# Performance work log

Hardware: AMD Instinct MI355X
Metric: run time of the kernel (lower is better)

The kernel has to match this reference:

```python
import jax, jax.numpy as jnp
import numpy as np

# dims: L = 1 + H*W tokens (cls first), BT = B*T clips*frames
L, BT, D = 577, 128, 768
B, T = 16, 8
H = W = 24
CM = 192   # d_middle = D // REDUCTION(4)
CR = 48    # CM // rf_r(4)
K = 3      # rf_k and spatial kernel


def setup_inputs() -> dict:
    key = jax.random.key(0)
    ks = jax.random.split(key, 10)
    return {
        "x":      jax.random.normal(ks[0], (L, BT, D), jnp.float32),
        # tada_pre_proj: Linear(D -> CM)
        "w_pre":  jax.random.normal(ks[1], (D, CM), jnp.float32) * 0.02,
        "b_pre":  jnp.zeros((CM,), jnp.float32),
        # TAdaConv2dV2 base depthwise weight (1x3x3, groups=CM) and bias
        "w_base": jax.random.normal(ks[2], (K, K, 1, CM), jnp.float32) * 0.1,
        "b_conv": jnp.zeros((CM,), jnp.float32),
        # route function: global 1x1 branch, temporal conv a (CM->CR), temporal conv b (CR->CM, small init)
        "w_g":    jax.random.normal(ks[3], (CM, CM), jnp.float32) * 0.02,
        "b_g":    jnp.zeros((CM,), jnp.float32),
        "w_a":    jax.random.normal(ks[4], (K, CM, CR), jnp.float32) * 0.05,
        "b_a":    jnp.zeros((CR,), jnp.float32),
        "w_b":    jax.random.normal(ks[5], (K, CR, CM), jnp.float32) * 0.02,
        # tada_proj: Linear(CM -> D)
        "w_proj": jax.random.normal(ks[6], (CM, D), jnp.float32) * 0.02,
        "b_proj": jnp.zeros((D,), jnp.float32),
    }


def reference(x, w_pre, b_pre, w_base, b_conv, w_g, b_g, w_a, b_a, w_b, w_proj, b_proj):
    # --- tada_pre_proj ---
    h = x @ w_pre + b_pre                                   # [L, BT, CM]
    cls_tok, sp = h[:1], h[1:]                              # cls token bypasses the conv
    sp = sp.transpose(1, 0, 2).reshape(BT, H, W, CM)        # [BT, H, W, CM]

    # --- route function: per-frame, per-channel calibration alpha ---
    d = sp.reshape(B, T, H * W, CM).mean(axis=2)            # spatial avg pool -> [B, T, CM]
    g = d.mean(axis=1) @ w_g + b_g                          # global temporal descriptor [B, CM]
    a = jax.lax.conv_general_dilated(d + g[:, None, :], w_a, (1,), 'SAME',
                                     dimension_numbers=('NWC', 'WIO', 'NWC')) + b_a
    a = jax.nn.relu(a)                                      # [B, T, CR]
    alpha = jax.lax.conv_general_dilated(a, w_b, (1,), 'SAME',
                                         dimension_numbers=('NWC', 'WIO', 'NWC')) + 1.0  # [B, T, CM]

    # --- calibrated depthwise conv (cal_dim='cout') ---
    # conv2d(x, alpha * W_base) == alpha * conv2d(x, W_base) for depthwise cout calibration
    y = jax.lax.conv_general_dilated(sp, w_base, (1, 1), 'SAME',
                                     dimension_numbers=('NHWC', 'HWIO', 'NHWC'),
                                     feature_group_count=CM)
    y = y * alpha.reshape(BT, 1, 1, CM) + b_conv            # [BT, H, W, CM]
    y = y.reshape(BT, H * W, CM).transpose(1, 0, 2)         # [HW, BT, CM]
    out = jnp.concatenate([cls_tok, y], axis=0)             # [L, BT, CM]

    # --- QuickGELU + tada_proj ---
    out = out * jax.nn.sigmoid(1.702 * out)
    return out @ w_proj + b_proj                            # [L, BT, D]
```

## Files before the change

kernel.cpp:

```cpp
#include <hip/hip_runtime.h>

#define DEV __device__ __forceinline__

typedef short bf16x8 __attribute__((ext_vector_type(8)));
typedef float f32x4  __attribute__((ext_vector_type(4)));
typedef unsigned short ushort_t;


DEV unsigned short f2bf(float f) {
  unsigned u = __float_as_uint(f);
  unsigned r = (u + 0x7fffu + ((u >> 16) & 1u)) >> 16;
  return (unsigned short)r;
}

DEV unsigned cvt_pk_bf16(float a, float b) {
  unsigned r;
  asm("v_cvt_pk_bf16_f32 %0, %1, %2" : "=v"(r) : "v"(a), "v"(b));
  return r;
}

DEV float bf2f(unsigned short b) { return __uint_as_float((unsigned)b << 16); }

DEV float silu_g(float v) { return v / (1.f + __expf(-1.702f * v)); }

DEV void gload_lds16(const void* g, void* l) {
  __builtin_amdgcn_global_load_lds(
      (const __attribute__((address_space(1))) unsigned int*)g,
      (__attribute__((address_space(3))) unsigned int*)l, 16, 0, 0);
}

__global__ __launch_bounds__(256)
void prep_kernel(const float* __restrict__ w_pre, const float* __restrict__ w_proj,
                 short* __restrict__ w_preT, short* __restrict__ w_projT) {
  int i = blockIdx.x * 256 + threadIdx.x;
  if (i < 192 * 768) {
    int n = i / 768, k = i - n * 768;
    w_preT[i] = (short)f2bf(w_pre[k * 192 + n]);
    int n2 = i / 192, k2 = i - n2 * 192;
    w_projT[i] = (short)f2bf(w_proj[k2 * 768 + n2]);
  }
}

__global__ __launch_bounds__(512, 4)
void gemm1_kernel(const float* __restrict__ Af, const short* __restrict__ Bt,
                  const float* __restrict__ bias, ushort_t* __restrict__ C) {
  constexpr int BM = 128, BN = 192, BK = 64, KTOT = 768, NTOT = 192, NT = 12;
  __shared__ short As[2][BM * BK];
  __shared__ short Bs[2][BN * BK];

  const int tid  = threadIdx.x;
  const int wave = tid >> 6, lane = tid & 63;
  const int m0 = blockIdx.x * BM;
  const int wm = wave >> 2, wn = wave & 3;
  const int lr  = lane & 15;
  const int lk8 = lane >> 4;
  const int srow = lane >> 3;
  const int schunk = lane & 7;

  f32x4 acc[4][3] = {};
  float4 areg[2][2];

  auto loadA_f32 = [&](int kt) {
    #pragma unroll
    for (int s = 0; s < 2; ++s) {
      int id = tid + s * 512;
      int r = id >> 3, c = id & 7;
      int cg = c ^ (r & 7);
      const float* p = Af + (size_t)(m0 + r) * KTOT + kt + cg * 8;
      areg[s][0] = *(const float4*)p;
      areg[s][1] = *(const float4*)(p + 4);
    }
  };
  auto cvtStoreA = [&](int buf) {
    #pragma unroll
    for (int s = 0; s < 2; ++s) {
      int id = tid + s * 512;
      int r = id >> 3, c = id & 7;
      int4 w;
      w.x = (int)cvt_pk_bf16(areg[s][0].x, areg[s][0].y);
      w.y = (int)cvt_pk_bf16(areg[s][0].z, areg[s][0].w);
      w.z = (int)cvt_pk_bf16(areg[s][1].x, areg[s][1].y);
      w.w = (int)cvt_pk_bf16(areg[s][1].z, areg[s][1].w);
      *(int4*)&As[buf][r * 64 + c * 8] = w;
    }
  };
  auto stageB = [&](int kt, int buf) {
    #pragma unroll
    for (int j = 0; j < 3; ++j) {
      int rb8 = wave * 3 + j;
      int r = rb8 * 8 + srow;
      const short* src = Bt + (size_t)r * KTOT + kt + (schunk ^ srow) * 8;
      gload_lds16(src, (char*)Bs[buf] + rb8 * 1024);
    }
  };
  auto compute = [&](int buf) {
    #pragma unroll
    for (int ks = 0; ks < 2; ++ks) {
      int kc = ks * 4 + lk8;
      bf16x8 af[4], bfv[3];
      #pragma unroll
      for (int fm = 0; fm < 4; ++fm) {
        int row = wm * 64 + fm * 16 + lr;
        af[fm] = *(const bf16x8*)&As[buf][row * 64 + (kc ^ (row & 7)) * 8];
      }
      #pragma unroll
      for (int fn = 0; fn < 3; ++fn) {
        int row = wn * 48 + fn * 16 + lr;
        bfv[fn] = *(const bf16x8*)&Bs[buf][row * 64 + (kc ^ (row & 7)) * 8];
      }
      #pragma unroll
      for (int fm = 0; fm < 4; ++fm)
        #pragma unroll
        for (int fn = 0; fn < 3; ++fn)
          acc[fm][fn] = __builtin_amdgcn_mfma_f32_16x16x32_bf16(
              bfv[fn], af[fm], acc[fm][fn], 0, 0, 0);
    }
  };

  loadA_f32(0);
  cvtStoreA(0);
  stageB(0, 0);
  loadA_f32(BK);
  asm volatile("s_waitcnt vmcnt(4) lgkmcnt(0)" ::: "memory");
  __builtin_amdgcn_s_barrier();

  #pragma unroll
  for (int t = 0; t < NT; ++t) {
    const int cur = t & 1, nxt = cur ^ 1;
    if (t + 1 < NT) {
      stageB((t + 1) * BK, nxt);
      cvtStoreA(nxt);
      if (t + 2 < NT) loadA_f32((t + 2) * BK);
    }
    compute(cur);
    if (t + 1 < NT) {
      if (t + 2 < NT)
        asm volatile("s_waitcnt vmcnt(4) lgkmcnt(0)" ::: "memory");
      else
        asm volatile("s_waitcnt vmcnt(0) lgkmcnt(0)" ::: "memory");
      __builtin_amdgcn_s_barrier();
    }
  }

  const int cb = (lane >> 4) * 4;
  #pragma unroll
  for (int fm = 0; fm < 4; ++fm) {
    int row = m0 + wm * 64 + fm * 16 + lr;
    #pragma unroll
    for (int fn = 0; fn < 3; ++fn) {
      int col = wn * 48 + fn * 16 + cb;
      float4 bv = *(const float4*)(bias + col);
      int2 w;
      w.x = (int)cvt_pk_bf16(acc[fm][fn][0] + bv.x, acc[fm][fn][1] + bv.y);
      w.y = (int)cvt_pk_bf16(acc[fm][fn][2] + bv.z, acc[fm][fn][3] + bv.w);
      *(int2*)&C[(size_t)row * NTOT + col] = w;
    }
  }
}

__global__ __launch_bounds__(512)
void gemm2_kernel(const short* __restrict__ Ab, const short* __restrict__ Bt,
                  const float* __restrict__ bias, float* __restrict__ C) {
  constexpr int BM = 128, BN = 192, BK = 64, KTOT = 192, NTOT = 768;
  __shared__ short As[3][BM * BK];
  __shared__ short Bs[3][BN * BK];

  const int tid  = threadIdx.x;
  const int wave = tid >> 6, lane = tid & 63;
  const int m0 = blockIdx.x * BM;
  const int n0 = blockIdx.y * BN;
  const int wm = wave >> 2, wn = wave & 3;
  const int lr  = lane & 15;
  const int lk8 = lane >> 4;
  const int srow = lane >> 3;
  const int schunk = lane & 7;

  f32x4 acc[4][3] = {};

  #pragma unroll
  for (int tt = 0; tt < 3; ++tt) {
    int kt = tt * BK;
    #pragma unroll
    for (int j = 0; j < 2; ++j) {
      int rb8 = wave * 2 + j;
      int r = rb8 * 8 + srow;
      const short* src = Ab + (size_t)(m0 + r) * KTOT + kt + (schunk ^ srow) * 8;
      gload_lds16(src, (char*)As[tt] + rb8 * 1024);
    }
    #pragma unroll
    for (int j = 0; j < 3; ++j) {
      int rb8 = wave * 3 + j;
      int r = rb8 * 8 + srow;
      const short* src = Bt + (size_t)(n0 + r) * KTOT + kt + (schunk ^ srow) * 8;
      gload_lds16(src, (char*)Bs[tt] + rb8 * 1024);
    }
  }

  auto compute = [&](int buf) {
    #pragma unroll
    for (int ks = 0; ks < 2; ++ks) {
      int kc = ks * 4 + lk8;
      bf16x8 af[4], bfv[3];
      #pragma unroll
      for (int fm = 0; fm < 4; ++fm) {
        int row = wm * 64 + fm * 16 + lr;
        af[fm] = *(const bf16x8*)&As[buf][row * 64 + (kc ^ (row & 7)) * 8];
      }
      #pragma unroll
      for (int fn = 0; fn < 3; ++fn) {
        int row = wn * 48 + fn * 16 + lr;
        bfv[fn] = *(const bf16x8*)&Bs[buf][row * 64 + (kc ^ (row & 7)) * 8];
      }
      #pragma unroll
      for (int fm = 0; fm < 4; ++fm)
        #pragma unroll
        for (int fn = 0; fn < 3; ++fn)
          acc[fm][fn] = __builtin_amdgcn_mfma_f32_16x16x32_bf16(
              bfv[fn], af[fm], acc[fm][fn], 0, 0, 0);
    }
  };

  asm volatile("s_waitcnt vmcnt(10)" ::: "memory");
  __builtin_amdgcn_s_barrier();
  compute(0);
  asm volatile("s_waitcnt vmcnt(5)" ::: "memory");
  __builtin_amdgcn_s_barrier();
  compute(1);
  asm volatile("s_waitcnt vmcnt(0)" ::: "memory");
  __builtin_amdgcn_s_barrier();
  compute(2);

  const int cb = (lane >> 4) * 4;
  #pragma unroll
  for (int fm = 0; fm < 4; ++fm) {
    int row = m0 + wm * 64 + fm * 16 + lr;
    #pragma unroll
    for (int fn = 0; fn < 3; ++fn) {
      int col = n0 + wn * 48 + fn * 16 + cb;
      float4 bv = *(const float4*)(bias + col);
      f32x4 o;
      o[0] = acc[fm][fn][0] + bv.x;
      o[1] = acc[fm][fn][1] + bv.y;
      o[2] = acc[fm][fn][2] + bv.z;
      o[3] = acc[fm][fn][3] + bv.w;
      __builtin_nontemporal_store(o, (f32x4*)&C[(size_t)row * NTOT + col]);
    }
  }
}

__global__ __launch_bounds__(384)
void reduce_d_kernel(const ushort_t* __restrict__ h, float* __restrict__ d) {
  const int bt = blockIdx.x, tid = threadIdx.x;
  const int slice = tid / 24, c8 = tid % 24;
  __shared__ float part[16][192];
  float sum[8] = {};
  #pragma unroll 4
  for (int i = 0; i < 36; ++i) {
    int l = 1 + slice * 36 + i;
    bf16x8 v = *(const bf16x8*)&h[((size_t)l * 128 + bt) * 192 + c8 * 8];
    #pragma unroll
    for (int j = 0; j < 8; ++j) sum[j] += bf2f((unsigned short)v[j]);
  }
  #pragma unroll
  for (int j = 0; j < 8; ++j) part[slice][c8 * 8 + j] = sum[j];
  __syncthreads();
  if (tid < 192) {
    float s = 0.f;
    #pragma unroll
    for (int sl = 0; sl < 16; ++sl) s += part[sl][tid];
    d[bt * 192 + tid] = s * (1.f / 576.f);
  }
}

__global__ __launch_bounds__(256)
void small_path_kernel(const float* __restrict__ d,
                       const float* __restrict__ w_g, const float* __restrict__ b_g,
                       const float* __restrict__ w_a, const float* __restrict__ b_a,
                       const float* __restrict__ w_b,
                       float* __restrict__ alpha) {
  const int b = blockIdx.x, tid = threadIdx.x;
  __shared__ unsigned short wg_buf[36864];
  __shared__ unsigned short wa_buf[27648];
  __shared__ float e[8][192];
  __shared__ float md[192];
  __shared__ float a[8][48];

  #pragma unroll
  for (int it = 0; it < 36; ++it) {
    int i = tid + it * 256;
    float4 v = *(const float4*)(w_g + i * 4);
    int2 w;
    w.x = (int)cvt_pk_bf16(v.x, v.y);
    w.y = (int)cvt_pk_bf16(v.z, v.w);
    *(int2*)&wg_buf[i * 4] = w;
  }
  #pragma unroll
  for (int it = 0; it < 27; ++it) {
    int i = tid + it * 256;
    float4 v = *(const float4*)(w_a + i * 4);
    int2 w;
    w.x = (int)cvt_pk_bf16(v.x, v.y);
    w.y = (int)cvt_pk_bf16(v.z, v.w);
    *(int2*)&wa_buf[i * 4] = w;
  }
  for (int i = tid; i < 384; i += 256)
    *(float4*)((float*)e + i * 4) = *(const float4*)(d + (size_t)b * 1536 + i * 4);
  __syncthreads();

  if (tid < 192) {
    float m = 0.f;
    #pragma unroll
    for (int t = 0; t < 8; ++t) m += e[t][tid];
    md[tid] = m * 0.125f;
  }
  __syncthreads();

  if (tid < 192) {
    float accg = b_g[tid];
    #pragma unroll 8
    for (int k = 0; k < 192; ++k)
      accg += md[k] * bf2f(wg_buf[k * 192 + tid]);
    #pragma unroll
    for (int t = 0; t < 8; ++t) e[t][tid] += accg;
  }
  __syncthreads();

  #pragma unroll
  for (int it = 0; it < 27; ++it) {
    int i = tid + it * 256;
    float4 v = *(const float4*)(w_b + i * 4);
    int2 w;
    w.x = (int)cvt_pk_bf16(v.x, v.y);
    w.y = (int)cvt_pk_bf16(v.z, v.w);
    *(int2*)&wg_buf[i * 4] = w;
  }
  for (int o = tid; o < 384; o += 256) {
    int t = o / 48, r = o - t * 48;
    float acc = b_a[r];
    #pragma unroll
    for (int dt = 0; dt < 3; ++dt) {
      int tt = t + dt - 1;
      if ((unsigned)tt < 8u) {
        #pragma unroll 8
        for (int k = 0; k < 192; ++k)
          acc += e[tt][k] * bf2f(wa_buf[(dt * 192 + k) * 48 + r]);
      }
    }
    a[t][r] = fmaxf(acc, 0.f);
  }
  __syncthreads();

  if (tid < 192) {
    #pragma unroll
    for (int t = 0; t < 8; ++t) {
      float acc = 1.0f;
      #pragma unroll
      for (int dt = 0; dt < 3; ++dt) {
        int tt = t + dt - 1;
        if ((unsigned)tt < 8u) {
          #pragma unroll 8
          for (int r = 0; r < 48; ++r)
            acc += a[tt][r] * bf2f(wg_buf[(dt * 48 + r) * 192 + tid]);
        }
      }
      alpha[(size_t)(b * 8 + t) * 192 + tid] = acc;
    }
  }
}

__global__ __launch_bounds__(256)
void dwconv_silu_kernel(const ushort_t* __restrict__ h, const float* __restrict__ alpha,
                        const float* __restrict__ w_base, const float* __restrict__ b_conv,
                        ushort_t* __restrict__ s) {
  const int bt = blockIdx.x, c0 = blockIdx.y * 32;
  const int tid = threadIdx.x;
  __shared__ ushort_t tile[576][32];

  #pragma unroll
  for (int it = 0; it < 9; ++it) {
    int gidx = tid + it * 256;
    int p = gidx >> 2, cc = (gidx & 3) * 8;
    *(bf16x8*)&tile[p][cc] =
        *(const bf16x8*)&h[((size_t)(1 + p) * 128 + bt) * 192 + c0 + cc];
  }

  const int c = tid & 31;
  const int prow = tid >> 5;
  float wv[3][3];
  #pragma unroll
  for (int dh = 0; dh < 3; ++dh)
    #pragma unroll
    for (int dw = 0; dw < 3; ++dw)
      wv[dh][dw] = w_base[(dh * 3 + dw) * 192 + c0 + c];
  const float av = alpha[bt * 192 + c0 + c];
  const float bc = b_conv[c0 + c];

  if (tid < 32) {
    float v = bf2f(h[(size_t)bt * 192 + c0 + tid]);
    s[(size_t)bt * 192 + c0 + tid] = f2bf(silu_g(v));
  }
  __syncthreads();

  for (int i = 0; i < 72; ++i) {
    int p = prow + i * 8;
    int hh = p / 24, ww = p - hh * 24;
    float acc = 0.f;
    #pragma unroll
    for (int dh = 0; dh < 3; ++dh) {
      int y = hh + dh - 1;
      if ((unsigned)y >= 24u) continue;
      #pragma unroll
      for (int dw = 0; dw < 3; ++dw) {
        int xx = ww + dw - 1;
        if ((unsigned)xx >= 24u) continue;
        acc += bf2f(tile[y * 24 + xx][c]) * wv[dh][dw];
      }
    }
    float pre = acc * av + bc;
    s[(size_t)((1 + p) * 128 + bt) * 192 + c0 + c] = f2bf(silu_g(pre));
  }
}

extern "C" void kernel_launch(void* const* d_in, const int* in_sizes, int n_in,
                              void* d_out, int out_size, void* d_ws, size_t ws_size,
                              hipStream_t stream) {
  (void)in_sizes; (void)n_in; (void)out_size; (void)ws_size;
  const float* x      = (const float*)d_in[0];
  const float* w_pre  = (const float*)d_in[1];
  const float* b_pre  = (const float*)d_in[2];
  const float* w_base = (const float*)d_in[3];
  const float* b_conv = (const float*)d_in[4];
  const float* w_g    = (const float*)d_in[5];
  const float* b_g    = (const float*)d_in[6];
  const float* w_a    = (const float*)d_in[7];
  const float* b_a    = (const float*)d_in[8];
  const float* w_b    = (const float*)d_in[9];
  const float* w_proj = (const float*)d_in[10];
  const float* b_proj = (const float*)d_in[11];

  float* out = (float*)d_out;
  ushort_t* h = (ushort_t*)d_out;
  char* ws = (char*)d_ws;
  short* w_preT  = (short*)(ws);
  short* w_projT = (short*)(ws + 294912);
  float* dbuf    = (float*)(ws + 589824);
  float* alpha   = (float*)(ws + 688128);
  short* s       = (short*)(ws + 786432);

  prep_kernel<<<576, 256, 0, stream>>>(w_pre, w_proj, w_preT, w_projT);

  gemm1_kernel<<<577, 512, 0, stream>>>(x, w_preT, b_pre, h);

  reduce_d_kernel<<<128, 384, 0, stream>>>(h, dbuf);
  small_path_kernel<<<16, 256, 0, stream>>>(dbuf, w_g, b_g, w_a, b_a, w_b, alpha);
  dwconv_silu_kernel<<<dim3(128, 6), 256, 0, stream>>>(h, alpha, w_base, b_conv,
                                                       (ushort_t*)s);

  gemm2_kernel<<<dim3(577, 4), 512, 0, stream>>>((const short*)s, w_projT,
                                                 b_proj, out);
}
```

Measured before the change: 250.7 us.

## Drop LDS staging in both GEMMs and load MFMA fragments directly from global

```diff
diff --git a/kernel.cpp b/kernel.cpp
--- a/kernel.cpp
+++ b/kernel.cpp
@@ -23,10 +23,15 @@
 
 DEV float silu_g(float v) { return v / (1.f + __expf(-1.702f * v)); }
 
-DEV void gload_lds16(const void* g, void* l) {
-  __builtin_amdgcn_global_load_lds(
-      (const __attribute__((address_space(1))) unsigned int*)g,
-      (__attribute__((address_space(3))) unsigned int*)l, 16, 0, 0);
+DEV bf16x8 loadA_cvt(const float* p) {
+  float4 v0 = *(const float4*)p;
+  float4 v1 = *(const float4*)(p + 4);
+  int4 w;
+  w.x = (int)cvt_pk_bf16(v0.x, v0.y);
+  w.y = (int)cvt_pk_bf16(v0.z, v0.w);
+  w.z = (int)cvt_pk_bf16(v1.x, v1.y);
+  w.w = (int)cvt_pk_bf16(v1.z, v1.w);
+  return __builtin_bit_cast(bf16x8, w);
 }
 
 __global__ __launch_bounds__(256)
@@ -41,105 +46,40 @@
   }
 }
 
-__global__ __launch_bounds__(512, 4)
+__global__ __launch_bounds__(512, 3)
 void gemm1_kernel(const float* __restrict__ Af, const short* __restrict__ Bt,
                   const float* __restrict__ bias, ushort_t* __restrict__ C) {
-  constexpr int BM = 128, BN = 192, BK = 64, KTOT = 768, NTOT = 192, NT = 12;
-  __shared__ short As[2][BM * BK];
-  __shared__ short Bs[2][BN * BK];
-
-  const int tid  = threadIdx.x;
+  constexpr int KTOT = 768, NTOT = 192, BM = 128;
+  const int tid = threadIdx.x;
   const int wave = tid >> 6, lane = tid & 63;
   const int m0 = blockIdx.x * BM;
   const int wm = wave >> 2, wn = wave & 3;
-  const int lr  = lane & 15;
-  const int lk8 = lane >> 4;
-  const int srow = lane >> 3;
-  const int schunk = lane & 7;
+  const int lr = lane & 15, lk8 = lane >> 4;
+
+  const float* aBase[4];
+  const short* bBase[3];
+  #pragma unroll
+  for (int fm = 0; fm < 4; ++fm)
+    aBase[fm] = Af + (size_t)(m0 + wm * 64 + fm * 16 + lr) * KTOT + lk8 * 8;
+  #pragma unroll
+  for (int fn = 0; fn < 3; ++fn)
+    bBase[fn] = Bt + (size_t)(wn * 48 + fn * 16 + lr) * KTOT + lk8 * 8;
 
   f32x4 acc[4][3] = {};
-  float4 areg[2][2];
-
-  auto loadA_f32 = [&](int kt) {
-    #pragma unroll
-    for (int s = 0; s < 2; ++s) {
-      int id = tid + s * 512;
-      int r = id >> 3, c = id & 7;
-      int cg = c ^ (r & 7);
-      const float* p = Af + (size_t)(m0 + r) * KTOT + kt + cg * 8;
-      areg[s][0] = *(const float4*)p;
-      areg[s][1] = *(const float4*)(p + 4);
-    }
-  };
-  auto cvtStoreA = [&](int buf) {
-    #pragma unroll
-    for (int s = 0; s < 2; ++s) {
-      int id = tid + s * 512;
-      int r = id >> 3, c = id & 7;
-      int4 w;
-      w.x = (int)cvt_pk_bf16(areg[s][0].x, areg[s][0].y);
-      w.y = (int)cvt_pk_bf16(areg[s][0].z, areg[s][0].w);
-      w.z = (int)cvt_pk_bf16(areg[s][1].x, areg[s][1].y);
-      w.w = (int)cvt_pk_bf16(areg[s][1].z, areg[s][1].w);
-      *(int4*)&As[buf][r * 64 + c * 8] = w;
-    }
-  };
-  auto stageB = [&](int kt, int buf) {
-    #pragma unroll
-    for (int j = 0; j < 3; ++j) {
-      int rb8 = wave * 3 + j;
-      int r = rb8 * 8 + srow;
-      const short* src = Bt + (size_t)r * KTOT + kt + (schunk ^ srow) * 8;
-      gload_lds16(src, (char*)Bs[buf] + rb8 * 1024);
-    }
-  };
-  auto compute = [&](int buf) {
-    #pragma unroll
-    for (int ks = 0; ks < 2; ++ks) {
-      int kc = ks * 4 + lk8;
-      bf16x8 af[4], bfv[3];
+
+  #pragma unroll 4
+  for (int kt = 0; kt < KTOT; kt += 32) {
+    bf16x8 af[4], bf[3];
+    #pragma unroll
+    for (int fm = 0; fm < 4; ++fm) af[fm] = loadA_cvt(aBase[fm] + kt);
+    #pragma unroll
+    for (int fn = 0; fn < 3; ++fn) bf[fn] = *(const bf16x8*)(bBase[fn] + kt);
+    #pragma unroll
+    for (int fm = 0; fm < 4; ++fm)
       #pragma unroll
-      for (int fm = 0; fm < 4; ++fm) {
-        int row = wm * 64 + fm * 16 + lr;
-        af[fm] = *(const bf16x8*)&As[buf][row * 64 + (kc ^ (row & 7)) * 8];
-      }
-      #pragma unroll
-      for (int fn = 0; fn < 3; ++fn) {
-        int row = wn * 48 + fn * 16 + lr;
-        bfv[fn] = *(const bf16x8*)&Bs[buf][row * 64 + (kc ^ (row & 7)) * 8];
-      }
-      #pragma unroll
-      for (int fm = 0; fm < 4; ++fm)
-        #pragma unroll
-        for (int fn = 0; fn < 3; ++fn)
-          acc[fm][fn] = __builtin_amdgcn_mfma_f32_16x16x32_bf16(
-              bfv[fn], af[fm], acc[fm][fn], 0, 0, 0);
-    }
-  };
-
-  loadA_f32(0);
-  cvtStoreA(0);
-  stageB(0, 0);
-  loadA_f32(BK);
-  asm volatile("s_waitcnt vmcnt(4) lgkmcnt(0)" ::: "memory");
-  __builtin_amdgcn_s_barrier();
-
-  #pragma unroll
-  for (int t = 0; t < NT; ++t) {
-    const int cur = t & 1, nxt = cur ^ 1;
-    if (t + 1 < NT) {
-      stageB((t + 1) * BK, nxt);
-      cvtStoreA(nxt);
-      if (t + 2 < NT) loadA_f32((t + 2) * BK);
-    }
-    compute(cur);
-    if (t + 1 < NT) {
-      if (t + 2 < NT)
-        asm volatile("s_waitcnt vmcnt(4) lgkmcnt(0)" ::: "memory");
-      else
-        asm volatile("s_waitcnt vmcnt(0) lgkmcnt(0)" ::: "memory");
-      __builtin_amdgcn_s_barrier();
-    }
+      for (int fn = 0; fn < 3; ++fn)
+        acc[fm][fn] = __builtin_amdgcn_mfma_f32_16x16x32_bf16(
+            bf[fn], af[fm], acc[fm][fn], 0, 0, 0);
   }
 
   const int cb = (lane >> 4) * 4;
@@ -158,77 +98,42 @@
   }
 }
 
-__global__ __launch_bounds__(512)
+__global__ __launch_bounds__(512, 4)
 void gemm2_kernel(const short* __restrict__ Ab, const short* __restrict__ Bt,
                   const float* __restrict__ bias, float* __restrict__ C) {
-  constexpr int BM = 128, BN = 192, BK = 64, KTOT = 192, NTOT = 768;
-  __shared__ short As[3][BM * BK];
-  __shared__ short Bs[3][BN * BK];
-
-  const int tid  = threadIdx.x;
+  constexpr int KTOT = 192, NTOT = 768, BM = 128;
+  const int tid = threadIdx.x;
   const int wave = tid >> 6, lane = tid & 63;
   const int m0 = blockIdx.x * BM;
-  const int n0 = blockIdx.y * BN;
+  const int n0 = blockIdx.y * 192;
   const int wm = wave >> 2, wn = wave & 3;
-  const int lr  = lane & 15;
-  const int lk8 = lane >> 4;
-  const int srow = lane >> 3;
-  const int schunk = lane & 7;
+  const int lr = lane & 15, lk8 = lane >> 4;
+
+  const short* aBase[4];
+  const short* bBase[3];
+  #pragma unroll
+  for (int fm = 0; fm < 4; ++fm)
+    aBase[fm] = Ab + (size_t)(m0 + wm * 64 + fm * 16 + lr) * KTOT + lk8 * 8;
+  #pragma unroll
+  for (int fn = 0; fn < 3; ++fn)
+    bBase[fn] = Bt + (size_t)(n0 + wn * 48 + fn * 16 + lr) * KTOT + lk8 * 8;
 
   f32x4 acc[4][3] = {};
 
   #pragma unroll
-  for (int tt = 0; tt < 3; ++tt) {
-    int kt = tt * BK;
-    #pragma unroll
-    for (int j = 0; j < 2; ++j) {
-      int rb8 = wave * 2 + j;
-      int r = rb8 * 8 + srow;
-      const short* src = Ab + (size_t)(m0 + r) * KTOT + kt + (schunk ^ srow) * 8;
-      gload_lds16(src, (char*)As[tt] + rb8 * 1024);
-    }
-    #pragma unroll
-    for (int j = 0; j < 3; ++j) {
-      int rb8 = wave * 3 + j;
-      int r = rb8 * 8 + srow;
-      const short* src = Bt + (size_t)(n0 + r) * KTOT + kt + (schunk ^ srow) * 8;
-      gload_lds16(src, (char*)Bs[tt] + rb8 * 1024);
-    }
-  }
-
-  auto compute = [&](int buf) {
-    #pragma unroll
-    for (int ks = 0; ks < 2; ++ks) {
-      int kc = ks * 4 + lk8;
-      bf16x8 af[4], bfv[3];
+  for (int kt = 0; kt < KTOT; kt += 32) {
+    bf16x8 af[4], bf[3];
+    #pragma unroll
+    for (int fm = 0; fm < 4; ++fm) af[fm] = *(const bf16x8*)(aBase[fm] + kt);
+    #pragma unroll
+    for (int fn = 0; fn < 3; ++fn) bf[fn] = *(const bf16x8*)(bBase[fn] + kt);
+    #pragma unroll
+    for (int fm = 0; fm < 4; ++fm)
       #pragma unroll
-      for (int fm = 0; fm < 4; ++fm) {
-        int row = wm * 64 + fm * 16 + lr;
-        af[fm] = *(const bf16x8*)&As[buf][row * 64 + (kc ^ (row & 7)) * 8];
-      }
-      #pragma unroll
-      for (int fn = 0; fn < 3; ++fn) {
-        int row = wn * 48 + fn * 16 + lr;
-        bfv[fn] = *(const bf16x8*)&Bs[buf][row * 64 + (kc ^ (row & 7)) * 8];
-      }
-      #pragma unroll
-      for (int fm = 0; fm < 4; ++fm)
-        #pragma unroll
-        for (int fn = 0; fn < 3; ++fn)
-          acc[fm][fn] = __builtin_amdgcn_mfma_f32_16x16x32_bf16(
-              bfv[fn], af[fm], acc[fm][fn], 0, 0, 0);
-    }
-  };
-
-  asm volatile("s_waitcnt vmcnt(10)" ::: "memory");
-  __builtin_amdgcn_s_barrier();
-  compute(0);
-  asm volatile("s_waitcnt vmcnt(5)" ::: "memory");
-  __builtin_amdgcn_s_barrier();
-  compute(1);
-  asm volatile("s_waitcnt vmcnt(0)" ::: "memory");
-  __builtin_amdgcn_s_barrier();
-  compute(2);
+      for (int fn = 0; fn < 3; ++fn)
+        acc[fm][fn] = __builtin_amdgcn_mfma_f32_16x16x32_bf16(
+            bf[fn], af[fm], acc[fm][fn], 0, 0, 0);
+  }
 
   const int cb = (lane >> 4) * 4;
   #pragma unroll
```

Result: slower. 413.8 us (+65.0%).

## Fuse depthwise conv, QuickGELU and output projection into one kernel

Applied to the files above, without the earlier changes.

```diff
diff --git a/kernel.cpp b/kernel.cpp
--- a/kernel.cpp
+++ b/kernel.cpp
@@ -44,9 +44,9 @@
 __global__ __launch_bounds__(512, 4)
 void gemm1_kernel(const float* __restrict__ Af, const short* __restrict__ Bt,
                   const float* __restrict__ bias, ushort_t* __restrict__ C) {
-  constexpr int BM = 128, BN = 192, BK = 64, KTOT = 768, NTOT = 192, NT = 12;
+  constexpr int BM = 128, BK = 64, KTOT = 768, NTOT = 192, NT = 12;
   __shared__ short As[2][BM * BK];
-  __shared__ short Bs[2][BN * BK];
+  __shared__ short Bs[2][192 * BK];
 
   const int tid  = threadIdx.x;
   const int wave = tid >> 6, lane = tid & 63;
@@ -154,96 +154,6 @@
       w.x = (int)cvt_pk_bf16(acc[fm][fn][0] + bv.x, acc[fm][fn][1] + bv.y);
       w.y = (int)cvt_pk_bf16(acc[fm][fn][2] + bv.z, acc[fm][fn][3] + bv.w);
       *(int2*)&C[(size_t)row * NTOT + col] = w;
-    }
-  }
-}
-
-__global__ __launch_bounds__(512)
-void gemm2_kernel(const short* __restrict__ Ab, const short* __restrict__ Bt,
-                  const float* __restrict__ bias, float* __restrict__ C) {
-  constexpr int BM = 128, BN = 192, BK = 64, KTOT = 192, NTOT = 768;
-  __shared__ short As[3][BM * BK];
-  __shared__ short Bs[3][BN * BK];
-
-  const int tid  = threadIdx.x;
-  const int wave = tid >> 6, lane = tid & 63;
-  const int m0 = blockIdx.x * BM;
-  const int n0 = blockIdx.y * BN;
-  const int wm = wave >> 2, wn = wave & 3;
-  const int lr  = lane & 15;
-  const int lk8 = lane >> 4;
-  const int srow = lane >> 3;
-  const int schunk = lane & 7;
-
-  f32x4 acc[4][3] = {};
-
-  #pragma unroll
-  for (int tt = 0; tt < 3; ++tt) {
-    int kt = tt * BK;
-    #pragma unroll
-    for (int j = 0; j < 2; ++j) {
-      int rb8 = wave * 2 + j;
-      int r = rb8 * 8 + srow;
-      const short* src = Ab + (size_t)(m0 + r) * KTOT + kt + (schunk ^ srow) * 8;
-      gload_lds16(src, (char*)As[tt] + rb8 * 1024);
-    }
-    #pragma unroll
-    for (int j = 0; j < 3; ++j) {
-      int rb8 = wave * 3 + j;
-      int r = rb8 * 8 + srow;
-      const short* src = Bt + (size_t)(n0 + r) * KTOT + kt + (schunk ^ srow) * 8;
-      gload_lds16(src, (char*)Bs[tt] + rb8 * 1024);
-    }
-  }
-
-  auto compute = [&](int buf) {
-    #pragma unroll
-    for (int ks = 0; ks < 2; ++ks) {
-      int kc = ks * 4 + lk8;
-      bf16x8 af[4], bfv[3];
-      #pragma unroll
-      for (int fm = 0; fm < 4; ++fm) {
-        int row = wm * 64 + fm * 16 + lr;
-        af[fm] = *(const bf16x8*)&As[buf][row * 64 + (kc ^ (row & 7)) * 8];
-      }
-      #pragma unroll
-      for (int fn = 0; fn < 3; ++fn) {
-        int row = wn * 48 + fn * 16 + lr;
-        bfv[fn] = *(const bf16x8*)&Bs[buf][row * 64 + (kc ^ (row & 7)) * 8];
-      }
-      #pragma unroll
-      for (int fm = 0; fm < 4; ++fm)
-        #pragma unroll
-        for (int fn = 0; fn < 3; ++fn)
-          acc[fm][fn] = __builtin_amdgcn_mfma_f32_16x16x32_bf16(
-              bfv[fn], af[fm], acc[fm][fn], 0, 0, 0);
-    }
-  };
-
-  asm volatile("s_waitcnt vmcnt(10)" ::: "memory");
-  __builtin_amdgcn_s_barrier();
-  compute(0);
-  asm volatile("s_waitcnt vmcnt(5)" ::: "memory");
-  __builtin_amdgcn_s_barrier();
-  compute(1);
-  asm volatile("s_waitcnt vmcnt(0)" ::: "memory");
-  __builtin_amdgcn_s_barrier();
-  compute(2);
-
-  const int cb = (lane >> 4) * 4;
-  #pragma unroll
-  for (int fm = 0; fm < 4; ++fm) {
-    int row = m0 + wm * 64 + fm * 16 + lr;
-    #pragma unroll
-    for (int fn = 0; fn < 3; ++fn) {
-      int col = n0 + wn * 48 + fn * 16 + cb;
-      float4 bv = *(const float4*)(bias + col);
-      f32x4 o;
-      o[0] = acc[fm][fn][0] + bv.x;
-      o[1] = acc[fm][fn][1] + bv.y;
-      o[2] = acc[fm][fn][2] + bv.z;
-      o[3] = acc[fm][fn][3] + bv.w;
-      __builtin_nontemporal_store(o, (f32x4*)&C[(size_t)row * NTOT + col]);
     }
   }
 }
@@ -368,56 +278,144 @@
   }
 }
 
-__global__ __launch_bounds__(256)
-void dwconv_silu_kernel(const ushort_t* __restrict__ h, const float* __restrict__ alpha,
-                        const float* __restrict__ w_base, const float* __restrict__ b_conv,
-                        ushort_t* __restrict__ s) {
-  const int bt = blockIdx.x, c0 = blockIdx.y * 32;
-  const int tid = threadIdx.x;
-  __shared__ ushort_t tile[576][32];
-
-  #pragma unroll
-  for (int it = 0; it < 9; ++it) {
-    int gidx = tid + it * 256;
-    int p = gidx >> 2, cc = (gidx & 3) * 8;
-    *(bf16x8*)&tile[p][cc] =
-        *(const bf16x8*)&h[((size_t)(1 + p) * 128 + bt) * 192 + c0 + cc];
-  }
-
-  const int c = tid & 31;
-  const int prow = tid >> 5;
-  float wv[3][3];
-  #pragma unroll
-  for (int dh = 0; dh < 3; ++dh)
-    #pragma unroll
-    for (int dw = 0; dw < 3; ++dw)
-      wv[dh][dw] = w_base[(dh * 3 + dw) * 192 + c0 + c];
-  const float av = alpha[bt * 192 + c0 + c];
-  const float bc = b_conv[c0 + c];
-
-  if (tid < 32) {
-    float v = bf2f(h[(size_t)bt * 192 + c0 + tid]);
-    s[(size_t)bt * 192 + c0 + tid] = f2bf(silu_g(v));
-  }
-  __syncthreads();
-
-  for (int i = 0; i < 72; ++i) {
-    int p = prow + i * 8;
-    int hh = p / 24, ww = p - hh * 24;
-    float acc = 0.f;
-    #pragma unroll
-    for (int dh = 0; dh < 3; ++dh) {
-      int y = hh + dh - 1;
-      if ((unsigned)y >= 24u) continue;
-      #pragma unroll
-      for (int dw = 0; dw < 3; ++dw) {
-        int xx = ww + dw - 1;
-        if ((unsigned)xx >= 24u) continue;
-        acc += bf2f(tile[y * 24 + xx][c]) * wv[dh][dw];
-      }
-    }
-    float pre = acc * av + bc;
-    s[(size_t)((1 + p) * 128 + bt) * 192 + c0 + c] = f2bf(silu_g(pre));
+__global__ __launch_bounds__(512, 2)
+void fused_out_kernel(const ushort_t* __restrict__ h, const float* __restrict__ alpha,
+                      const float* __restrict__ w_base, const float* __restrict__ b_conv,
+                      const short* __restrict__ Bt, const float* __restrict__ bias,
+                      float* __restrict__ out) {
+  constexpr int KTOT = 192, NTOT = 768;
+  __shared__ ushort_t Stile[128 * 192];
+  __shared__ short    Btile[192 * 192];
+
+  const int tid  = threadIdx.x;
+  const int blk  = blockIdx.x;
+  const int wave = tid >> 6, lane = tid & 63;
+  const int wm = wave >> 2, wn = wave & 3;
+  const int lr = lane & 15, lk8 = lane >> 4;
+
+  const int row = tid >> 2;
+  const int cg  = tid & 3;
+  if (blk == 0) {
+    #pragma unroll
+    for (int j = 0; j < 6; ++j) {
+      int c8 = cg + 4 * j;
+      bf16x8 hv = *(const bf16x8*)&h[(size_t)row * 192 + c8 * 8];
+      int4 pk;
+      float v0 = silu_g(bf2f((ushort_t)hv[0])), v1 = silu_g(bf2f((ushort_t)hv[1]));
+      float v2 = silu_g(bf2f((ushort_t)hv[2])), v3 = silu_g(bf2f((ushort_t)hv[3]));
+      float v4 = silu_g(bf2f((ushort_t)hv[4])), v5 = silu_g(bf2f((ushort_t)hv[5]));
+      float v6 = silu_g(bf2f((ushort_t)hv[6])), v7 = silu_g(bf2f((ushort_t)hv[7]));
+      pk.x = (int)cvt_pk_bf16(v0, v1); pk.y = (int)cvt_pk_bf16(v2, v3);
+      pk.z = (int)cvt_pk_bf16(v4, v5); pk.w = (int)cvt_pk_bf16(v6, v7);
+      int chp = (c8 & ~7) | ((c8 & 7) ^ (row & 7));
+      *(int4*)&Stile[row * 192 + chp * 8] = pk;
+    }
+  } else {
+    const int p = blk - 1, hh = p / 24, ww = p - hh * 24;
+    #pragma unroll
+    for (int j = 0; j < 6; ++j) {
+      int c8 = cg + 4 * j;
+      int cbase = c8 * 8;
+      float acc8[8] = {};
+      #pragma unroll
+      for (int dh = 0; dh < 3; ++dh) {
+        int y = hh + dh - 1;
+        if ((unsigned)y >= 24u) continue;
+        #pragma unroll
+        for (int dw = 0; dw < 3; ++dw) {
+          int xx = ww + dw - 1;
+          if ((unsigned)xx >= 24u) continue;
+          bf16x8 hv = *(const bf16x8*)
+              &h[((size_t)(1 + y * 24 + xx) * 128 + row) * 192 + cbase];
+          const float* wp = w_base + (dh * 3 + dw) * 192 + cbase;
+          float4 w0 = *(const float4*)wp, w1 = *(const float4*)(wp + 4);
+          acc8[0] += bf2f((ushort_t)hv[0]) * w0.x;
+          acc8[1] += bf2f((ushort_t)hv[1]) * w0.y;
+          acc8[2] += bf2f((ushort_t)hv[2]) * w0.z;
+          acc8[3] += bf2f((ushort_t)hv[3]) * w0.w;
+          acc8[4] += bf2f((ushort_t)hv[4]) * w1.x;
+          acc8[5] += bf2f((ushort_t)hv[5]) * w1.y;
+          acc8[6] += bf2f((ushort_t)hv[6]) * w1.z;
+          acc8[7] += bf2f((ushort_t)hv[7]) * w1.w;
+        }
+      }
+      const float* ap = alpha + (size_t)row * 192 + cbase;
+      float4 a0 = *(const float4*)ap, a1 = *(const float4*)(ap + 4);
+      const float* bp = b_conv + cbase;
+      float4 c0 = *(const float4*)bp, c1 = *(const float4*)(bp + 4);
+      float v0 = silu_g(acc8[0] * a0.x + c0.x), v1 = silu_g(acc8[1] * a0.y + c0.y);
+      float v2 = silu_g(acc8[2] * a0.z + c0.z), v3 = silu_g(acc8[3] * a0.w + c0.w);
+      float v4 = silu_g(acc8[4] * a1.x + c1.x), v5 = silu_g(acc8[5] * a1.y + c1.y);
+      float v6 = silu_g(acc8[6] * a1.z + c1.z), v7 = silu_g(acc8[7] * a1.w + c1.w);
+      int4 pk;
+      pk.x = (int)cvt_pk_bf16(v0, v1); pk.y = (int)cvt_pk_bf16(v2, v3);
+      pk.z = (int)cvt_pk_bf16(v4, v5); pk.w = (int)cvt_pk_bf16(v6, v7);
+      int chp = (c8 & ~7) | ((c8 & 7) ^ (row & 7));
+      *(int4*)&Stile[row * 192 + chp * 8] = pk;
+    }
+  }
+
+  #pragma unroll 1
+  for (int nc = 0; nc < 4; ++nc) {
+    const int n0 = nc * 192;
+    __syncthreads();
+
+    #pragma unroll
+    for (int i = 0; i < 9; ++i) {
+      int q = wave * 576 + i * 64 + lane;
+      int brow = q / 24;
+      int ch = q - brow * 24;
+      int ach = (ch & ~7) | ((ch & 7) ^ (brow & 7));
+      const short* src = Bt + (size_t)(n0 + brow) * KTOT + ach * 8;
+      gload_lds16(src, (char*)Btile + (wave * 9 + i) * 1024);
+    }
+    asm volatile("s_waitcnt vmcnt(0)" ::: "memory");
+    __builtin_amdgcn_s_barrier();
+
+    f32x4 acc[4][3] = {};
+    #pragma unroll
+    for (int kt = 0; kt < 3; ++kt) {
+      #pragma unroll
+      for (int ks = 0; ks < 2; ++ks) {
+        int kc = kt * 8 + ks * 4 + lk8;
+        bf16x8 af[4], bfv[3];
+        #pragma unroll
+        for (int fm = 0; fm < 4; ++fm) {
+          int sr = wm * 64 + fm * 16 + lr;
+          int chp = (kc & ~7) | ((kc & 7) ^ (sr & 7));
+          af[fm] = *(const bf16x8*)&Stile[sr * 192 + chp * 8];
+        }
+        #pragma unroll
+        for (int fn = 0; fn < 3; ++fn) {
+          int br = wn * 48 + fn * 16 + lr;
+          int chp = (kc & ~7) | ((kc & 7) ^ (br & 7));
+          bfv[fn] = *(const bf16x8*)&Btile[br * 192 + chp * 8];
+        }
+        #pragma unroll
+        for (int fm = 0; fm < 4; ++fm)
+          #pragma unroll
+          for (int fn = 0; fn < 3; ++fn)
+            acc[fm][fn] = __builtin_amdgcn_mfma_f32_16x16x32_bf16(
+                bfv[fn], af[fm], acc[fm][fn], 0, 0, 0);
+      }
+    }
+
+    const int cb = (lane >> 4) * 4;
+    #pragma unroll
+    for (int fm = 0; fm < 4; ++fm) {
+      int orow = blk * 128 + wm * 64 + fm * 16 + lr;
+      #pragma unroll
+      for (int fn = 0; fn < 3; ++fn) {
+        int col = n0 + wn * 48 + fn * 16 + cb;
+        float4 bv = *(const float4*)(bias + col);
+        f32x4 o;
+        o[0] = acc[fm][fn][0] + bv.x;
+        o[1] = acc[fm][fn][1] + bv.y;
+        o[2] = acc[fm][fn][2] + bv.z;
+        o[3] = acc[fm][fn][3] + bv.w;
+        __builtin_nontemporal_store(o, (f32x4*)&out[(size_t)orow * NTOT + col]);
+      }
+    }
   }
 }
 
@@ -439,13 +437,12 @@
   const float* b_proj = (const float*)d_in[11];
 
   float* out = (float*)d_out;
-  ushort_t* h = (ushort_t*)d_out;
   char* ws = (char*)d_ws;
   short* w_preT  = (short*)(ws);
   short* w_projT = (short*)(ws + 294912);
   float* dbuf    = (float*)(ws + 589824);
   float* alpha   = (float*)(ws + 688128);
-  short* s       = (short*)(ws + 786432);
+  ushort_t* h    = (ushort_t*)(ws + 786432);
 
   prep_kernel<<<576, 256, 0, stream>>>(w_pre, w_proj, w_preT, w_projT);
 
@@ -453,9 +450,7 @@
 
   reduce_d_kernel<<<128, 384, 0, stream>>>(h, dbuf);
   small_path_kernel<<<16, 256, 0, stream>>>(dbuf, w_g, b_g, w_a, b_a, w_b, alpha);
-  dwconv_silu_kernel<<<dim3(128, 6), 256, 0, stream>>>(h, alpha, w_base, b_conv,
-                                                       (ushort_t*)s);
-
-  gemm2_kernel<<<dim3(577, 4), 512, 0, stream>>>((const short*)s, w_projT,
-                                                 b_proj, out);
-}
+
+  fused_out_kernel<<<577, 512, 0, stream>>>(h, alpha, w_base, b_conv,
+                                            w_projT, b_proj, out);
+}
```

Result: faster. 241.3 us (-3.8%).

## Restructure gemm2 to stage the activation tile once and loop over N chunks

Applied to the files above, without the earlier changes.

```diff
diff --git a/kernel.cpp b/kernel.cpp
--- a/kernel.cpp
+++ b/kernel.cpp
@@ -44,9 +44,9 @@
 __global__ __launch_bounds__(512, 4)
 void gemm1_kernel(const float* __restrict__ Af, const short* __restrict__ Bt,
                   const float* __restrict__ bias, ushort_t* __restrict__ C) {
-  constexpr int BM = 128, BN = 192, BK = 64, KTOT = 768, NTOT = 192, NT = 12;
+  constexpr int BM = 128, BK = 64, KTOT = 768, NTOT = 192, NT = 12;
   __shared__ short As[2][BM * BK];
-  __shared__ short Bs[2][BN * BK];
+  __shared__ short Bs[2][192 * BK];
 
   const int tid  = threadIdx.x;
   const int wave = tid >> 6, lane = tid & 63;
@@ -154,96 +154,6 @@
       w.x = (int)cvt_pk_bf16(acc[fm][fn][0] + bv.x, acc[fm][fn][1] + bv.y);
       w.y = (int)cvt_pk_bf16(acc[fm][fn][2] + bv.z, acc[fm][fn][3] + bv.w);
       *(int2*)&C[(size_t)row * NTOT + col] = w;
-    }
-  }
-}
-
-__global__ __launch_bounds__(512)
-void gemm2_kernel(const short* __restrict__ Ab, const short* __restrict__ Bt,
-                  const float* __restrict__ bias, float* __restrict__ C) {
-  constexpr int BM = 128, BN = 192, BK = 64, KTOT = 192, NTOT = 768;
-  __shared__ short As[3][BM * BK];
-  __shared__ short Bs[3][BN * BK];
-
-  const int tid  = threadIdx.x;
-  const int wave = tid >> 6, lane = tid & 63;
-  const int m0 = blockIdx.x * BM;
-  const int n0 = blockIdx.y * BN;
-  const int wm = wave >> 2, wn = wave & 3;
-  const int lr  = lane & 15;
-  const int lk8 = lane >> 4;
-  const int srow = lane >> 3;
-  const int schunk = lane & 7;
-
-  f32x4 acc[4][3] = {};
-
-  #pragma unroll
-  for (int tt = 0; tt < 3; ++tt) {
-    int kt = tt * BK;
-    #pragma unroll
-    for (int j = 0; j < 2; ++j) {
-      int rb8 = wave * 2 + j;
-      int r = rb8 * 8 + srow;
-      const short* src = Ab + (size_t)(m0 + r) * KTOT + kt + (schunk ^ srow) * 8;
-      gload_lds16(src, (char*)As[tt] + rb8 * 1024);
-    }
-    #pragma unroll
-    for (int j = 0; j < 3; ++j) {
-      int rb8 = wave * 3 + j;
-      int r = rb8 * 8 + srow;
-      const short* src = Bt + (size_t)(n0 + r) * KTOT + kt + (schunk ^ srow) * 8;
-      gload_lds16(src, (char*)Bs[tt] + rb8 * 1024);
-    }
-  }
-
-  auto compute = [&](int buf) {
-    #pragma unroll
-    for (int ks = 0; ks < 2; ++ks) {
-      int kc = ks * 4 + lk8;
-      bf16x8 af[4], bfv[3];
-      #pragma unroll
-      for (int fm = 0; fm < 4; ++fm) {
-        int row = wm * 64 + fm * 16 + lr;
-        af[fm] = *(const bf16x8*)&As[buf][row * 64 + (kc ^ (row & 7)) * 8];
-      }
-      #pragma unroll
-      for (int fn = 0; fn < 3; ++fn) {
-        int row = wn * 48 + fn * 16 + lr;
-        bfv[fn] = *(const bf16x8*)&Bs[buf][row * 64 + (kc ^ (row & 7)) * 8];
-      }
-      #pragma unroll
-      for (int fm = 0; fm < 4; ++fm)
-        #pragma unroll
-        for (int fn = 0; fn < 3; ++fn)
-          acc[fm][fn] = __builtin_amdgcn_mfma_f32_16x16x32_bf16(
-              bfv[fn], af[fm], acc[fm][fn], 0, 0, 0);
-    }
-  };
-
-  asm volatile("s_waitcnt vmcnt(10)" ::: "memory");
-  __builtin_amdgcn_s_barrier();
-  compute(0);
-  asm volatile("s_waitcnt vmcnt(5)" ::: "memory");
-  __builtin_amdgcn_s_barrier();
-  compute(1);
-  asm volatile("s_waitcnt vmcnt(0)" ::: "memory");
-  __builtin_amdgcn_s_barrier();
-  compute(2);
-
-  const int cb = (lane >> 4) * 4;
-  #pragma unroll
-  for (int fm = 0; fm < 4; ++fm) {
-    int row = m0 + wm * 64 + fm * 16 + lr;
-    #pragma unroll
-    for (int fn = 0; fn < 3; ++fn) {
-      int col = n0 + wn * 48 + fn * 16 + cb;
-      float4 bv = *(const float4*)(bias + col);
-      f32x4 o;
-      o[0] = acc[fm][fn][0] + bv.x;
-      o[1] = acc[fm][fn][1] + bv.y;
-      o[2] = acc[fm][fn][2] + bv.z;
-      o[3] = acc[fm][fn][3] + bv.w;
-      __builtin_nontemporal_store(o, (f32x4*)&C[(size_t)row * NTOT + col]);
     }
   }
 }
@@ -369,9 +279,9 @@
 }
 
 __global__ __launch_bounds__(256)
-void dwconv_silu_kernel(const ushort_t* __restrict__ h, const float* __restrict__ alpha,
+void dwconv_silu_kernel(const ushort_t* h, const float* __restrict__ alpha,
                         const float* __restrict__ w_base, const float* __restrict__ b_conv,
-                        ushort_t* __restrict__ s) {
+                        ushort_t* s) {
   const int bt = blockIdx.x, c0 = blockIdx.y * 32;
   const int tid = threadIdx.x;
   __shared__ ushort_t tile[576][32];
@@ -418,6 +328,76 @@
     }
     float pre = acc * av + bc;
     s[(size_t)((1 + p) * 128 + bt) * 192 + c0 + c] = f2bf(silu_g(pre));
+  }
+}
+
+__global__ __launch_bounds__(512, 4)
+void gemm2_kernel(const ushort_t* __restrict__ s, const short* __restrict__ Bt,
+                  const float* __restrict__ bias, float* __restrict__ out) {
+  constexpr int KTOT = 192, NTOT = 768;
+  __shared__ ushort_t Stile[128 * 192];
+
+  const int tid  = threadIdx.x;
+  const int l    = blockIdx.x;
+  const int wave = tid >> 6, lane = tid & 63;
+  const int wm = wave >> 2, wn = wave & 3;
+  const int lr = lane & 15, lk8 = lane >> 4;
+
+  #pragma unroll
+  for (int i = 0; i < 6; ++i) {
+    int q = wave * 384 + i * 64 + lane;
+    int row = q / 24;
+    int ch = q - row * 24;
+    int ach = (ch & ~7) | ((ch & 7) ^ (row & 7));
+    const ushort_t* src = s + ((size_t)l * 128 + row) * KTOT + ach * 8;
+    gload_lds16(src, (char*)Stile + (wave * 6 + i) * 1024);
+  }
+  asm volatile("s_waitcnt vmcnt(0)" ::: "memory");
+  __builtin_amdgcn_s_barrier();
+
+  const int cb = (lane >> 4) * 4;
+  #pragma unroll 1
+  for (int nc = 0; nc < 4; ++nc) {
+    const int n0 = nc * 192;
+    f32x4 acc[4][3] = {};
+    #pragma unroll
+    for (int kt = 0; kt < 6; ++kt) {
+      bf16x8 bfv[3];
+      #pragma unroll
+      for (int fn = 0; fn < 3; ++fn)
+        bfv[fn] = *(const bf16x8*)(Bt +
+            (size_t)(n0 + wn * 48 + fn * 16 + lr) * KTOT + kt * 32 + lk8 * 8);
+      bf16x8 af[4];
+      #pragma unroll
+      for (int fm = 0; fm < 4; ++fm) {
+        int sr = wm * 64 + fm * 16 + lr;
+        int kc = kt * 4 + lk8;
+        int chp = (kc & ~7) | ((kc & 7) ^ (sr & 7));
+        af[fm] = *(const bf16x8*)&Stile[sr * 192 + chp * 8];
+      }
+      #pragma unroll
+      for (int fm = 0; fm < 4; ++fm)
+        #pragma unroll
+        for (int fn = 0; fn < 3; ++fn)
+          acc[fm][fn] = __builtin_amdgcn_mfma_f32_16x16x32_bf16(
+              bfv[fn], af[fm], acc[fm][fn], 0, 0, 0);
+    }
+
+    #pragma unroll
+    for (int fm = 0; fm < 4; ++fm) {
+      int orow = l * 128 + wm * 64 + fm * 16 + lr;
+      #pragma unroll
+      for (int fn = 0; fn < 3; ++fn) {
+        int col = n0 + wn * 48 + fn * 16 + cb;
+        float4 bv = *(const float4*)(bias + col);
+        f32x4 o;
+        o[0] = acc[fm][fn][0] + bv.x;
+        o[1] = acc[fm][fn][1] + bv.y;
+        o[2] = acc[fm][fn][2] + bv.z;
+        o[3] = acc[fm][fn][3] + bv.w;
+        __builtin_nontemporal_store(o, (f32x4*)&out[(size_t)orow * NTOT + col]);
+      }
+    }
   }
 }
 
@@ -439,13 +419,12 @@
   const float* b_proj = (const float*)d_in[11];
 
   float* out = (float*)d_out;
-  ushort_t* h = (ushort_t*)d_out;
   char* ws = (char*)d_ws;
   short* w_preT  = (short*)(ws);
   short* w_projT = (short*)(ws + 294912);
   float* dbuf    = (float*)(ws + 589824);
   float* alpha   = (float*)(ws + 688128);
-  short* s       = (short*)(ws + 786432);
+  ushort_t* h    = (ushort_t*)(ws + 786432);
 
   prep_kernel<<<576, 256, 0, stream>>>(w_pre, w_proj, w_preT, w_projT);
 
@@ -453,9 +432,8 @@
 
   reduce_d_kernel<<<128, 384, 0, stream>>>(h, dbuf);
   small_path_kernel<<<16, 256, 0, stream>>>(dbuf, w_g, b_g, w_a, b_a, w_b, alpha);
-  dwconv_silu_kernel<<<dim3(128, 6), 256, 0, stream>>>(h, alpha, w_base, b_conv,
-                                                       (ushort_t*)s);
-
-  gemm2_kernel<<<dim3(577, 4), 512, 0, stream>>>((const short*)s, w_projT,
-                                                 b_proj, out);
-}
+
+  dwconv_silu_kernel<<<dim3(128, 6), 256, 0, stream>>>(h, alpha, w_base, b_conv, h);
+
+  gemm2_kernel<<<577, 512, 0, stream>>>(h, w_projT, b_proj, out);
+}
```

Measured after the change: 336.0 us. +34.0%, slower.
